# Optimization experiments

Hardware: AMD Instinct MI355X
Metric: run time of the kernel (lower is better)

The kernel has to match this reference:

```python
import jax, jax.numpy as jnp
import numpy as np

EPS = 1e-5

def layer_norm(x, gamma, beta):
    m = jnp.mean(x, axis=-1, keepdims=True)
    v = jnp.var(x, axis=-1, keepdims=True)
    return (x - m) * jax.lax.rsqrt(v + EPS) * gamma + beta


def setup_inputs() -> dict:
    key = jax.random.key(0)
    ks = jax.random.split(key, 8)
    B, N, E, C = 1, 512, 128, 128
    s = 0.02
    inp = {
        "pair_rep": jax.random.normal(ks[0], (B, N, N, E), dtype=jnp.float32),
        "ln_pair_g": jnp.ones((E,), jnp.float32),
        "ln_pair_b": jnp.zeros((E,), jnp.float32),
        "ga_w": jax.random.normal(ks[1], (E, C), jnp.float32) * s,
        "ga_b": jnp.zeros((C,), jnp.float32),
        "la_w": jax.random.normal(ks[2], (E, C), jnp.float32) * s,
        "la_b": jnp.zeros((C,), jnp.float32),
        "gb_w": jax.random.normal(ks[3], (E, C), jnp.float32) * s,
        "gb_b": jnp.zeros((C,), jnp.float32),
        "lb_w": jax.random.normal(ks[4], (E, C), jnp.float32) * s,
        "lb_b": jnp.zeros((C,), jnp.float32),
        "g_w": jax.random.normal(ks[5], (E, E), jnp.float32) * s,
        "g_b": jnp.zeros((E,), jnp.float32),
        "ln_up_g": jnp.ones((C,), jnp.float32),
        "ln_up_b": jnp.zeros((C,), jnp.float32),
        "lu_w": jax.random.normal(ks[6], (C, E), jnp.float32) * s,
        "lu_b": jnp.zeros((E,), jnp.float32),
    }
    return inp


def reference(pair_rep, ln_pair_g, ln_pair_b, ga_w, ga_b, la_w, la_b,
              gb_w, gb_b, lb_w, lb_b, g_w, g_b, ln_up_g, ln_up_b, lu_w, lu_b):
    # pair_rep: [B, N, N, E]
    z = layer_norm(pair_rep, ln_pair_g, ln_pair_b)
    a = jax.nn.sigmoid(z @ ga_w + ga_b) * (z @ la_w + la_b)  # [B,N,N,C]
    b = jax.nn.sigmoid(z @ gb_w + gb_b) * (z @ lb_w + lb_b)  # [B,N,N,C]
    g = jax.nn.sigmoid(z @ g_w + g_b)                        # [B,N,N,E]
    # torch: sum(a.unsqueeze(-3)*b.unsqueeze(-4), dim=-2) == sum_k a[i,k,c]*b[j,k,c]
    update = jnp.einsum("bikc,bjkc->bijc", a, b)             # [B,N,N,C]
    out = g * (layer_norm(update, ln_up_g, ln_up_b) @ lu_w + lu_b)
    return out
```

## Files before the change

### kernel.cpp

```cpp
#include <hip/hip_runtime.h>
#include <hip/hip_bf16.h>

#define NN 512
#define MM (NN*NN)

typedef __attribute__((ext_vector_type(8))) unsigned short u16x8;
typedef __attribute__((ext_vector_type(4))) unsigned short u16x4;
typedef __attribute__((ext_vector_type(8))) __bf16 bf16x8;
typedef __attribute__((ext_vector_type(4))) float f32x4;

static __device__ __forceinline__ unsigned short f2bfi(float f) {
  return __builtin_bit_cast(unsigned short, __float2bfloat16(f));
}
static __device__ __forceinline__ float bf2f(unsigned short h) {
  return __uint_as_float(((unsigned int)h) << 16);
}
static __device__ __forceinline__ bf16x8 ldfrag(const unsigned short* p) {
  u16x8 v = *(const u16x8*)p;
  return __builtin_bit_cast(bf16x8, v);
}
static __device__ __forceinline__ float sigm(float x) {
  return __builtin_amdgcn_rcpf(1.0f + __expf(-x));
}

__global__ void prep_weights(const float* __restrict__ ga_w, const float* __restrict__ la_w,
                             const float* __restrict__ gb_w, const float* __restrict__ lb_w,
                             const float* __restrict__ g_w,  const float* __restrict__ lu_w,
                             unsigned short* __restrict__ WT) {
  int idx = blockIdx.x * 256 + threadIdx.x;
  if (idx >= 768 * 128) return;
  int n = idx >> 7;
  int k = idx & 127;
  int grp = n >> 7, cn = n & 127;
  const float* tabs[6] = {ga_w, la_w, gb_w, lb_w, g_w, lu_w};
  WT[idx] = f2bfi(tabs[grp][k * 128 + cn]);
}

__global__ __launch_bounds__(512, 4) void k1_proj(
    const float* __restrict__ pair, const float* __restrict__ lng, const float* __restrict__ lnb,
    const unsigned short* __restrict__ WT,
    const float* __restrict__ ga_b, const float* __restrict__ la_b,
    const float* __restrict__ gb_b, const float* __restrict__ lb_b,
    const float* __restrict__ g_b,
    unsigned short* __restrict__ a_t, unsigned short* __restrict__ b_t,
    unsigned short* __restrict__ g_buf) {
  __shared__ __align__(16) unsigned short W0[128 * 136];
  __shared__ __align__(16) unsigned short W1[128 * 136];
  const int t = threadIdx.x;
  const size_t m0 = (size_t)blockIdx.x * 128;
  const int wave = t >> 6, lane = t & 63, lrow = lane & 15, qk = lane >> 4;
  const int rbase = t >> 4, off_ = (t & 15) * 8;

  u16x8 rga[4], rla[4], rgb[4], rlb[4], rg[4];
  auto stage_ld = [&](u16x8* r, int base) {
#pragma unroll
    for (int it = 0; it < 4; ++it)
      r[it] = *(const u16x8*)(WT + (size_t)(base + it * 32 + rbase) * 128 + off_);
  };
  auto stage_st = [&](unsigned short* buf, const u16x8* r) {
#pragma unroll
    for (int it = 0; it < 4; ++it)
      *(u16x8*)(buf + (it * 32 + rbase) * 136 + off_) = r[it];
  };

  stage_ld(rga, 0);
  stage_ld(rla, 128);

  {
    const int row = t >> 2, q = t & 3;
    const float* pr = pair + (m0 + row) * 128 + q * 32;
    float vals[32];
    float s = 0.f, ss = 0.f;
#pragma unroll
    for (int it = 0; it < 8; ++it) {
      f32x4 v = *(const f32x4*)(pr + it * 4);
#pragma unroll
      for (int j = 0; j < 4; ++j) { float x = v[j]; vals[it * 4 + j] = x; s += x; ss += x * x; }
    }
    s += __shfl_xor(s, 1);  s += __shfl_xor(s, 2);
    ss += __shfl_xor(ss, 1); ss += __shfl_xor(ss, 2);
    const float mean = s * (1.f / 128.f);
    const float var  = ss * (1.f / 128.f) - mean * mean;
    const float rstd = rsqrtf(var + 1e-5f);
#pragma unroll
    for (int i = 0; i < 4; ++i) {
      u16x8 pk;
#pragma unroll
      for (int j = 0; j < 8; ++j) {
        int c = q * 32 + i * 8 + j;
        pk[j] = f2bfi((vals[i * 8 + j] - mean) * rstd * lng[c] + lnb[c]);
      }
      *(u16x8*)(W0 + row * 136 + q * 32 + i * 8) = pk;
    }
  }
  __syncthreads();

  bf16x8 af[4];
  f32x4 accg[8], accl[8];
  auto run_gemm = [&](const unsigned short* buf, f32x4* acc) {
#pragma unroll
    for (int nt = 0; nt < 8; ++nt)
#pragma unroll
      for (int r = 0; r < 4; ++r) acc[nt][r] = 0.f;
#pragma unroll
    for (int ks = 0; ks < 4; ++ks)
#pragma unroll
      for (int nt = 0; nt < 8; ++nt) {
        bf16x8 bv = ldfrag(buf + (nt * 16 + lrow) * 136 + ks * 32 + 8 * qk);
        acc[nt] = __builtin_amdgcn_mfma_f32_16x16x32_bf16(af[ks], bv, acc[nt], 0, 0, 0);
      }
  };
  auto epi_ab = [&](unsigned short* buf, const float* gbias, const float* lbias) {
#pragma unroll
    for (int nt = 0; nt < 8; ++nt) {
      int col = nt * 16 + lrow;
      float bg = gbias[col], bl = lbias[col];
      u16x4 pk;
#pragma unroll
      for (int r = 0; r < 4; ++r)
        pk[r] = f2bfi(sigm(accg[nt][r] + bg) * (accl[nt][r] + bl));
      *(u16x4*)(buf + col * 136 + wave * 16 + qk * 4) = pk;
    }
  };
  auto wout = [&](unsigned short* dst, const unsigned short* buf) {
#pragma unroll
    for (int it = 0; it < 4; ++it) {
      int idx = it * 512 + t;
      int col = idx >> 4, i = idx & 15;
      *(u16x8*)(dst + (size_t)col * MM + m0 + i * 8) = *(const u16x8*)(buf + col * 136 + i * 8);
    }
  };

#pragma unroll
  for (int ks = 0; ks < 4; ++ks)
    af[ks] = ldfrag(W0 + (wave * 16 + lrow) * 136 + ks * 32 + 8 * qk);
  stage_st(W1, rga);
  stage_ld(rgb, 256);
  __syncthreads();
  run_gemm(W1, accg);
  stage_st(W0, rla);
  stage_ld(rlb, 384);
  __syncthreads();
  run_gemm(W0, accl);
  stage_st(W1, rgb);
  stage_ld(rg, 512);
  __syncthreads();
  epi_ab(W0, ga_b, la_b);
  __syncthreads();
  wout(a_t, W0);
  run_gemm(W1, accg);
  __syncthreads();
  stage_st(W0, rlb);
  stage_st(W1, rg);
  __syncthreads();
  run_gemm(W0, accl);
  __syncthreads();
  epi_ab(W0, gb_b, lb_b);
  run_gemm(W1, accg);
  __syncthreads();
  wout(b_t, W0);
#pragma unroll
  for (int nt = 0; nt < 8; ++nt) {
    int col = nt * 16 + lrow;
    float bg = g_b[col];
#pragma unroll
    for (int r = 0; r < 4; ++r)
      W1[(wave * 16 + qk * 4 + r) * 136 + col] = f2bfi(sigm(accg[nt][r] + bg));
  }
  __syncthreads();
#pragma unroll
  for (int it = 0; it < 4; ++it) {
    int idx = it * 512 + t;
    int mr = idx >> 4, off = (idx & 15) * 8;
    *(u16x8*)(g_buf + (m0 + mr) * 128 + off) = *(const u16x8*)(W1 + mr * 136 + off);
  }
}

__global__ __launch_bounds__(256) void k2_einsum(
    const unsigned short* __restrict__ a_t, const unsigned short* __restrict__ b_t,
    unsigned short* __restrict__ up_t) {
  __shared__ __align__(16) unsigned short lds[20480];
  const int t = threadIdx.x;
  const int wid = (blockIdx.x & 7) * 256 + (blockIdx.x >> 3);
  const int c = wid >> 4;
  const int i0 = ((wid >> 2) & 3) * 128, j0 = (wid & 3) * 128;
  const unsigned short* Ag = a_t + (size_t)c * MM + (size_t)i0 * 512;
  const unsigned short* Bg = b_t + (size_t)c * MM + (size_t)j0 * 512;
  const int wave = t >> 6, lane = t & 63, wr = wave >> 1, wc = wave & 1;
  const int lrow = lane & 15, qk = lane >> 4;
  const int srow = t >> 2, sq = t & 3;
  f32x4 acc[4][4];
#pragma unroll
  for (int i = 0; i < 4; ++i)
#pragma unroll
    for (int j = 0; j < 4; ++j)
#pragma unroll
      for (int r = 0; r < 4; ++r) acc[i][j][r] = 0.f;

  u16x8 ra[2], rb[2];
  auto tile_ld = [&](int k0) {
#pragma unroll
    for (int h = 0; h < 2; ++h) {
      int row = h * 64 + srow;
      ra[h] = *(const u16x8*)(Ag + (size_t)row * 512 + k0 + sq * 8);
      rb[h] = *(const u16x8*)(Bg + (size_t)row * 512 + k0 + sq * 8);
    }
  };
  auto tile_st = [&](int buf) {
    unsigned short* sA = lds + buf * 5120;
    unsigned short* sB = lds + 10240 + buf * 5120;
#pragma unroll
    for (int h = 0; h < 2; ++h) {
      int row = h * 64 + srow;
      *(u16x8*)(sA + row * 40 + sq * 8) = ra[h];
      *(u16x8*)(sB + row * 40 + sq * 8) = rb[h];
    }
  };

  tile_ld(0);
  tile_st(0);
  __syncthreads();
  int cur = 0;
  for (int ks = 0; ks < 16; ++ks) {
    if (ks < 15) tile_ld((ks + 1) * 32);
    const unsigned short* sA = lds + cur * 5120;
    const unsigned short* sB = lds + 10240 + cur * 5120;
    bf16x8 afr[4], bv[4];
#pragma unroll
    for (int mt = 0; mt < 4; ++mt)
      afr[mt] = ldfrag(sA + (wr * 64 + mt * 16 + lrow) * 40 + 8 * qk);
#pragma unroll
    for (int nt = 0; nt < 4; ++nt)
      bv[nt] = ldfrag(sB + (wc * 64 + nt * 16 + lrow) * 40 + 8 * qk);
#pragma unroll
    for (int mt = 0; mt < 4; ++mt)
#pragma unroll
      for (int nt = 0; nt < 4; ++nt)
        acc[mt][nt] = __builtin_amdgcn_mfma_f32_16x16x32_bf16(afr[mt], bv[nt], acc[mt][nt], 0, 0, 0);
    if (ks < 15) tile_st(cur ^ 1);
    __syncthreads();
    cur ^= 1;
  }
  unsigned short* sC = lds;
#pragma unroll
  for (int mt = 0; mt < 4; ++mt)
#pragma unroll
    for (int nt = 0; nt < 4; ++nt) {
      int col = wc * 64 + nt * 16 + lrow;
#pragma unroll
      for (int r = 0; r < 4; ++r) {
        int row = wr * 64 + mt * 16 + qk * 4 + r;
        sC[row * 136 + col] = f2bfi(acc[mt][nt][r]);
      }
    }
  __syncthreads();
  unsigned short* up = up_t + (size_t)c * MM;
#pragma unroll
  for (int it = 0; it < 8; ++it) {
    int idx = it * 256 + t;
    int row = idx >> 4, q = idx & 15;
    *(u16x8*)(up + (size_t)(i0 + row) * 512 + j0 + q * 8) = *(const u16x8*)(sC + row * 136 + q * 8);
  }
}

__global__ __launch_bounds__(256) void k3_final(
    const unsigned short* __restrict__ up_t, const unsigned short* __restrict__ g_buf,
    const unsigned short* __restrict__ WT,
    const float* __restrict__ lnug, const float* __restrict__ lnub,
    const float* __restrict__ lu_b, float* __restrict__ out) {
  __shared__ __align__(16) unsigned short sU[64 * 138];
  __shared__ __align__(16) unsigned short sA[64 * 136];
  __shared__ __align__(16) unsigned short sB[128 * 136];
  const int t = threadIdx.x;
  const size_t m0 = (size_t)blockIdx.x * 64;
#pragma unroll
  for (int it = 0; it < 4; ++it) {
    int idx = it * 256 + t;
    int c = idx >> 3, m8 = (idx & 7) * 8;
    u16x8 v = *(const u16x8*)(up_t + (size_t)c * MM + m0 + m8);
#pragma unroll
    for (int j = 0; j < 8; ++j) sU[(m8 + j) * 138 + c] = v[j];
  }
#pragma unroll
  for (int it = 0; it < 8; ++it) {
    int idx = it * 256 + t;
    int n = idx >> 4, off = (idx & 15) * 8;
    *(u16x8*)(sB + n * 136 + off) = *(const u16x8*)(WT + (size_t)(640 + n) * 128 + off);
  }
  __syncthreads();
  {
    const int row = t >> 2, q = t & 3;
    float vals[32]; float s = 0.f, ss = 0.f;
#pragma unroll
    for (int jj = 0; jj < 32; ++jj) {
      int cc = q + jj * 4;
      float x = bf2f(sU[row * 138 + cc]);
      vals[jj] = x; s += x; ss += x * x;
    }
    s += __shfl_xor(s, 1);  s += __shfl_xor(s, 2);
    ss += __shfl_xor(ss, 1); ss += __shfl_xor(ss, 2);
    float mean = s * (1.f / 128.f);
    float var  = ss * (1.f / 128.f) - mean * mean;
    float rstd = rsqrtf(var + 1e-5f);
#pragma unroll
    for (int jj = 0; jj < 32; ++jj) {
      int cc = q + jj * 4;
      float zn = (vals[jj] - mean) * rstd * lnug[cc] + lnub[cc];
      sA[row * 136 + cc] = f2bfi(zn);
    }
  }
  __syncthreads();
  const int wave = t >> 6, lane = t & 63, lrow = lane & 15, qk = lane >> 4;
  f32x4 acc[8];
#pragma unroll
  for (int i = 0; i < 8; ++i)
#pragma unroll
    for (int r = 0; r < 4; ++r) acc[i][r] = 0.f;
#pragma unroll
  for (int ks = 0; ks < 4; ++ks) {
    int k0 = ks * 32;
    bf16x8 af = ldfrag(sA + (wave * 16 + lrow) * 136 + k0 + 8 * qk);
#pragma unroll
    for (int nt = 0; nt < 8; ++nt) {
      bf16x8 bv = ldfrag(sB + (nt * 16 + lrow) * 136 + k0 + 8 * qk);
      acc[nt] = __builtin_amdgcn_mfma_f32_16x16x32_bf16(af, bv, acc[nt], 0, 0, 0);
    }
  }
#pragma unroll
  for (int nt = 0; nt < 8; ++nt) {
    int e = nt * 16 + lrow;
    float bb = lu_b[e];
#pragma unroll
    for (int r = 0; r < 4; ++r) {
      size_t m = m0 + wave * 16 + qk * 4 + r;
      float lin = acc[nt][r] + bb;
      float gv = bf2f(g_buf[m * 128 + e]);
      out[m * 128 + e] = gv * lin;
    }
  }
}

extern "C" void kernel_launch(void* const* d_in, const int* in_sizes, int n_in,
                              void* d_out, int out_size, void* d_ws, size_t ws_size,
                              hipStream_t stream) {
  const float* pair = (const float*)d_in[0];
  const float* lng  = (const float*)d_in[1];
  const float* lnb  = (const float*)d_in[2];
  const float* ga_w = (const float*)d_in[3];
  const float* ga_b = (const float*)d_in[4];
  const float* la_w = (const float*)d_in[5];
  const float* la_b = (const float*)d_in[6];
  const float* gb_w = (const float*)d_in[7];
  const float* gb_b = (const float*)d_in[8];
  const float* lb_w = (const float*)d_in[9];
  const float* lb_b = (const float*)d_in[10];
  const float* g_w  = (const float*)d_in[11];
  const float* g_b  = (const float*)d_in[12];
  const float* lnug = (const float*)d_in[13];
  const float* lnub = (const float*)d_in[14];
  const float* lu_w = (const float*)d_in[15];
  const float* lu_b = (const float*)d_in[16];
  float* out = (float*)d_out;

  char* ws = (char*)d_ws;
  unsigned short* WT    = (unsigned short*)(ws);
  unsigned short* a_t   = (unsigned short*)(ws + 196608ull);
  unsigned short* b_t   = (unsigned short*)(ws + 67305472ull);
  unsigned short* g_buf = (unsigned short*)(ws + 134414336ull);
  unsigned short* up_t  = (unsigned short*)(ws + 201523200ull);

  hipLaunchKernelGGL(prep_weights, dim3(384), dim3(256), 0, stream,
                     ga_w, la_w, gb_w, lb_w, g_w, lu_w, WT);
  hipLaunchKernelGGL(k1_proj, dim3(2048), dim3(512), 0, stream,
                     pair, lng, lnb, WT, ga_b, la_b, gb_b, lb_b, g_b, a_t, b_t, g_buf);
  hipLaunchKernelGGL(k2_einsum, dim3(2048), dim3(256), 0, stream, a_t, b_t, up_t);
  hipLaunchKernelGGL(k3_final, dim3(4096), dim3(256), 0, stream,
                     up_t, g_buf, WT, lnug, lnub, lu_b, out);
}
```

Before: 291.1 us.

## Stream pre-swizzled weights into LDS via global_load_lds and retile k1 waves

prep_weights now also writes a pre-swizzled bf16 copy of the five projection weights, which k1 loads directly into LDS with global_load_lds instead of staging them through registers. The B-fragment reads use an XOR swizzle to avoid bank conflicts without padding. k1's wave tiling changes from 8x1 to 4x2 (32 rows by 64 columns per wave), so each B fragment feeds two MFMAs. k2 drops the LDS-staged output and writes scalar bf16 values straight to global memory, which removes a barrier but produces less coalesced stores.

Result: slower. 340.8 us (+17.1%).

```diff
diff --git a/kernel.cpp b/kernel.cpp
--- a/kernel.cpp
+++ b/kernel.cpp
@@ -26,19 +26,27 @@
 __global__ void prep_weights(const float* __restrict__ ga_w, const float* __restrict__ la_w,
                              const float* __restrict__ gb_w, const float* __restrict__ lb_w,
                              const float* __restrict__ g_w,  const float* __restrict__ lu_w,
-                             unsigned short* __restrict__ WT) {
+                             unsigned short* __restrict__ WT, unsigned short* __restrict__ WTs) {
   int idx = blockIdx.x * 256 + threadIdx.x;
-  if (idx >= 768 * 128) return;
-  int n = idx >> 7;
-  int k = idx & 127;
-  int grp = n >> 7, cn = n & 127;
   const float* tabs[6] = {ga_w, la_w, gb_w, lb_w, g_w, lu_w};
-  WT[idx] = f2bfi(tabs[grp][k * 128 + cn]);
+  if (idx < 98304) {
+    int n = idx >> 7, k = idx & 127;
+    int grp = n >> 7, cn = n & 127;
+    WT[idx] = f2bfi(tabs[grp][k * 128 + cn]);
+  } else {
+    int id2 = idx - 98304;
+    int gm = id2 >> 14;
+    int r2 = id2 & 16383;
+    int row = r2 >> 7, s = r2 & 127;
+    int pchunk = s >> 3, j = s & 7;
+    int k = ((pchunk ^ (row & 15)) << 3) + j;
+    WTs[id2] = f2bfi(tabs[gm][k * 128 + row]);
+  }
 }
 
 __global__ __launch_bounds__(512, 4) void k1_proj(
     const float* __restrict__ pair, const float* __restrict__ lng, const float* __restrict__ lnb,
-    const unsigned short* __restrict__ WT,
+    const unsigned short* __restrict__ WTs,
     const float* __restrict__ ga_b, const float* __restrict__ la_b,
     const float* __restrict__ gb_b, const float* __restrict__ lb_b,
     const float* __restrict__ g_b,
@@ -49,22 +57,18 @@
   const int t = threadIdx.x;
   const size_t m0 = (size_t)blockIdx.x * 128;
   const int wave = t >> 6, lane = t & 63, lrow = lane & 15, qk = lane >> 4;
-  const int rbase = t >> 4, off_ = (t & 15) * 8;
-
-  u16x8 rga[4], rla[4], rgb[4], rlb[4], rg[4];
-  auto stage_ld = [&](u16x8* r, int base) {
-#pragma unroll
-    for (int it = 0; it < 4; ++it)
-      r[it] = *(const u16x8*)(WT + (size_t)(base + it * 32 + rbase) * 128 + off_);
-  };
-  auto stage_st = [&](unsigned short* buf, const u16x8* r) {
-#pragma unroll
-    for (int it = 0; it < 4; ++it)
-      *(u16x8*)(buf + (it * 32 + rbase) * 136 + off_) = r[it];
-  };
-
-  stage_ld(rga, 0);
-  stage_ld(rla, 128);
+  const int wr = wave >> 1, wc = wave & 1;
+
+  auto stage_g = [&](unsigned short* buf, int gm) {
+    const unsigned short* src = WTs + gm * 16384 + wave * 512 + lane * 8;
+    unsigned short* dst = buf + wave * 512;
+#pragma unroll
+    for (int cc = 0; cc < 4; ++cc)
+      __builtin_amdgcn_global_load_lds((const void*)(src + cc * 4096),
+                                       (void*)(dst + cc * 4096), 16, 0, 0);
+  };
+
+  stage_g(W1, 0);
 
   {
     const int row = t >> 2, q = t & 3;
@@ -95,32 +99,45 @@
   }
   __syncthreads();
 
-  bf16x8 af[4];
-  f32x4 accg[8], accl[8];
-  auto run_gemm = [&](const unsigned short* buf, f32x4* acc) {
-#pragma unroll
-    for (int nt = 0; nt < 8; ++nt)
-#pragma unroll
-      for (int r = 0; r < 4; ++r) acc[nt][r] = 0.f;
+  bf16x8 af[2][4];
+#pragma unroll
+  for (int mi = 0; mi < 2; ++mi)
 #pragma unroll
     for (int ks = 0; ks < 4; ++ks)
-#pragma unroll
-      for (int nt = 0; nt < 8; ++nt) {
-        bf16x8 bv = ldfrag(buf + (nt * 16 + lrow) * 136 + ks * 32 + 8 * qk);
-        acc[nt] = __builtin_amdgcn_mfma_f32_16x16x32_bf16(af[ks], bv, acc[nt], 0, 0, 0);
+      af[mi][ks] = ldfrag(W0 + (wr * 32 + mi * 16 + lrow) * 136 + ks * 32 + 8 * qk);
+  __syncthreads();
+
+  f32x4 accg[2][4], accl[2][4];
+  auto run_gemm = [&](const unsigned short* buf, f32x4 (*acc)[4]) {
+#pragma unroll
+    for (int mi = 0; mi < 2; ++mi)
+#pragma unroll
+      for (int nt = 0; nt < 4; ++nt)
+#pragma unroll
+        for (int r = 0; r < 4; ++r) acc[mi][nt][r] = 0.f;
+#pragma unroll
+    for (int ks = 0; ks < 4; ++ks)
+#pragma unroll
+      for (int nt = 0; nt < 4; ++nt) {
+        int rr = wc * 64 + nt * 16 + lrow;
+        bf16x8 bv = ldfrag(buf + rr * 128 + (((ks * 4 + qk) ^ lrow) * 8));
+        acc[0][nt] = __builtin_amdgcn_mfma_f32_16x16x32_bf16(af[0][ks], bv, acc[0][nt], 0, 0, 0);
+        acc[1][nt] = __builtin_amdgcn_mfma_f32_16x16x32_bf16(af[1][ks], bv, acc[1][nt], 0, 0, 0);
       }
   };
   auto epi_ab = [&](unsigned short* buf, const float* gbias, const float* lbias) {
 #pragma unroll
-    for (int nt = 0; nt < 8; ++nt) {
-      int col = nt * 16 + lrow;
-      float bg = gbias[col], bl = lbias[col];
-      u16x4 pk;
-#pragma unroll
-      for (int r = 0; r < 4; ++r)
-        pk[r] = f2bfi(sigm(accg[nt][r] + bg) * (accl[nt][r] + bl));
-      *(u16x4*)(buf + col * 136 + wave * 16 + qk * 4) = pk;
-    }
+    for (int mi = 0; mi < 2; ++mi)
+#pragma unroll
+      for (int nt = 0; nt < 4; ++nt) {
+        int col = wc * 64 + nt * 16 + lrow;
+        float bg = gbias[col], bl = lbias[col];
+        u16x4 pk;
+#pragma unroll
+        for (int r = 0; r < 4; ++r)
+          pk[r] = f2bfi(sigm(accg[mi][nt][r] + bg) * (accl[mi][nt][r] + bl));
+        *(u16x4*)(buf + col * 136 + wr * 32 + mi * 16 + qk * 4) = pk;
+      }
   };
   auto wout = [&](unsigned short* dst, const unsigned short* buf) {
 #pragma unroll
@@ -131,27 +148,19 @@
     }
   };
 
-#pragma unroll
-  for (int ks = 0; ks < 4; ++ks)
-    af[ks] = ldfrag(W0 + (wave * 16 + lrow) * 136 + ks * 32 + 8 * qk);
-  stage_st(W1, rga);
-  stage_ld(rgb, 256);
-  __syncthreads();
   run_gemm(W1, accg);
-  stage_st(W0, rla);
-  stage_ld(rlb, 384);
+  stage_g(W0, 1);
   __syncthreads();
   run_gemm(W0, accl);
-  stage_st(W1, rgb);
-  stage_ld(rg, 512);
+  stage_g(W1, 2);
   __syncthreads();
   epi_ab(W0, ga_b, la_b);
   __syncthreads();
   wout(a_t, W0);
   run_gemm(W1, accg);
   __syncthreads();
-  stage_st(W0, rlb);
-  stage_st(W1, rg);
+  stage_g(W0, 3);
+  stage_g(W1, 4);
   __syncthreads();
   run_gemm(W0, accl);
   __syncthreads();
@@ -160,13 +169,15 @@
   __syncthreads();
   wout(b_t, W0);
 #pragma unroll
-  for (int nt = 0; nt < 8; ++nt) {
-    int col = nt * 16 + lrow;
-    float bg = g_b[col];
-#pragma unroll
-    for (int r = 0; r < 4; ++r)
-      W1[(wave * 16 + qk * 4 + r) * 136 + col] = f2bfi(sigm(accg[nt][r] + bg));
-  }
+  for (int mi = 0; mi < 2; ++mi)
+#pragma unroll
+    for (int nt = 0; nt < 4; ++nt) {
+      int col = wc * 64 + nt * 16 + lrow;
+      float bg = g_b[col];
+#pragma unroll
+      for (int r = 0; r < 4; ++r)
+        W1[(wr * 32 + mi * 16 + qk * 4 + r) * 136 + col] = f2bfi(sigm(accg[mi][nt][r] + bg));
+    }
   __syncthreads();
 #pragma unroll
   for (int it = 0; it < 4; ++it) {
@@ -241,26 +252,18 @@
     __syncthreads();
     cur ^= 1;
   }
-  unsigned short* sC = lds;
+  unsigned short* up = up_t + (size_t)c * MM;
 #pragma unroll
   for (int mt = 0; mt < 4; ++mt)
 #pragma unroll
     for (int nt = 0; nt < 4; ++nt) {
-      int col = wc * 64 + nt * 16 + lrow;
+      int col = j0 + wc * 64 + nt * 16 + lrow;
 #pragma unroll
       for (int r = 0; r < 4; ++r) {
-        int row = wr * 64 + mt * 16 + qk * 4 + r;
-        sC[row * 136 + col] = f2bfi(acc[mt][nt][r]);
+        int row = i0 + wr * 64 + mt * 16 + qk * 4 + r;
+        up[(size_t)row * 512 + col] = f2bfi(acc[mt][nt][r]);
       }
     }
-  __syncthreads();
-  unsigned short* up = up_t + (size_t)c * MM;
-#pragma unroll
-  for (int it = 0; it < 8; ++it) {
-    int idx = it * 256 + t;
-    int row = idx >> 4, q = idx & 15;
-    *(u16x8*)(up + (size_t)(i0 + row) * 512 + j0 + q * 8) = *(const u16x8*)(sC + row * 136 + q * 8);
-  }
 }
 
 __global__ __launch_bounds__(256) void k3_final(
@@ -364,15 +367,16 @@
 
   char* ws = (char*)d_ws;
   unsigned short* WT    = (unsigned short*)(ws);
-  unsigned short* a_t   = (unsigned short*)(ws + 196608ull);
-  unsigned short* b_t   = (unsigned short*)(ws + 67305472ull);
-  unsigned short* g_buf = (unsigned short*)(ws + 134414336ull);
-  unsigned short* up_t  = (unsigned short*)(ws + 201523200ull);
-
-  hipLaunchKernelGGL(prep_weights, dim3(384), dim3(256), 0, stream,
-                     ga_w, la_w, gb_w, lb_w, g_w, lu_w, WT);
+  unsigned short* WTs   = (unsigned short*)(ws + 196608ull);
+  unsigned short* a_t   = (unsigned short*)(ws + 360448ull);
+  unsigned short* b_t   = (unsigned short*)(ws + 67469312ull);
+  unsigned short* g_buf = (unsigned short*)(ws + 134578176ull);
+  unsigned short* up_t  = (unsigned short*)(ws + 201687040ull);
+
+  hipLaunchKernelGGL(prep_weights, dim3(704), dim3(256), 0, stream,
+                     ga_w, la_w, gb_w, lb_w, g_w, lu_w, WT, WTs);
   hipLaunchKernelGGL(k1_proj, dim3(2048), dim3(512), 0, stream,
-                     pair, lng, lnb, WT, ga_b, la_b, gb_b, lb_b, g_b, a_t, b_t, g_buf);
+                     pair, lng, lnb, WTs, ga_b, la_b, gb_b, lb_b, g_b, a_t, b_t, g_buf);
   hipLaunchKernelGGL(k2_einsum, dim3(2048), dim3(256), 0, stream, a_t, b_t, up_t);
   hipLaunchKernelGGL(k3_final, dim3(4096), dim3(256), 0, stream,
                      up_t, g_buf, WT, lnug, lnub, lu_b, out);
```
